# Optimization experiments

Hardware: AMD Instinct MI355X
Metric: run time of the kernel (lower is better)

Reference implementation:

```python
import jax, jax.numpy as jnp
import numpy as np

H = 16          # num heads
DH = 64         # head dim
D = H * DH      # hidden = 1024


def setup_inputs() -> dict:
    key = jax.random.key(0)
    ks = jax.random.split(key, 9)
    s = 1.0 / np.sqrt(D)
    return {
        "hidden_states": jax.random.normal(ks[0], (4, 2048, D), dtype=jnp.float32),
        "Wq": jax.random.normal(ks[1], (D, D), dtype=jnp.float32) * s,
        "bq": jax.random.normal(ks[2], (D,), dtype=jnp.float32) * 0.02,
        "Wk": jax.random.normal(ks[3], (D, D), dtype=jnp.float32) * s,
        "bk": jax.random.normal(ks[4], (D,), dtype=jnp.float32) * 0.02,
        "Wv": jax.random.normal(ks[5], (D, D), dtype=jnp.float32) * s,
        "bv": jax.random.normal(ks[6], (D,), dtype=jnp.float32) * 0.02,
        "Wo": jax.random.normal(ks[7], (D, D), dtype=jnp.float32) * s,
        "bo": jax.random.normal(ks[8], (D,), dtype=jnp.float32) * 0.02,
    }


def _split_heads(x):  # [B,S,D] -> [B,H,S,DH]
    B, S, _ = x.shape
    return x.reshape(B, S, H, DH).transpose(0, 2, 1, 3)


def reference(hidden_states, Wq, bq, Wk, bk, Wv, bv, Wo, bo):
    # torch Linear: y = x @ W.T + b  (W stored as [out, in])
    q = _split_heads(jnp.einsum('bsd,ed->bse', hidden_states, Wq) + bq)
    k = _split_heads(jnp.einsum('bsd,ed->bse', hidden_states, Wk) + bk)
    v = _split_heads(jnp.einsum('bsd,ed->bse', hidden_states, Wv) + bv)
    scores = jnp.einsum('bhqd,bhkd->bhqk', q, k) / np.sqrt(DH)
    probs = jax.nn.softmax(scores, axis=-1)  # fused softmax+matmul in original
    ctx = jnp.einsum('bhqk,bhkd->bhqd', probs, v)
    B, _, S, _ = ctx.shape
    ctx = ctx.transpose(0, 2, 1, 3).reshape(B, S, D)
    out = jnp.einsum('bsd,ed->bse', ctx, Wo) + bo
    return out  # weights are None (vis=False); dropout rate asserted 0
```

## Files before the change

kernel.cpp:

```cpp
#include <hip/hip_runtime.h>


typedef __bf16 bf16;
typedef __bf16 bf16x8 __attribute__((ext_vector_type(8)));
typedef __bf16 bf16x4 __attribute__((ext_vector_type(4)));
typedef float  floatx4 __attribute__((ext_vector_type(4)));

#define NB   4
#define SEQ  2048
#define NH   16
#define DH   64
#define DIM  1024
#define MTOT (NB * SEQ)

#define CEXP 0.18033688f

__device__ __forceinline__ floatx4 zero4() {
    floatx4 z; z[0] = 0.f; z[1] = 0.f; z[2] = 0.f; z[3] = 0.f; return z;
}

__device__ __forceinline__ void load_lds16(const bf16* g, bf16* l) {
    __builtin_amdgcn_global_load_lds(
        (__attribute__((address_space(1))) void*)g,
        (__attribute__((address_space(3))) void*)l,
        16, 0, 0);
}

__global__ __launch_bounds__(256) void cvt_all(const float* __restrict__ X,
                                               const float* __restrict__ w0,
                                               const float* __restrict__ w1,
                                               const float* __restrict__ w2,
                                               const float* __restrict__ w3,
                                               bf16* __restrict__ Xb,
                                               bf16* __restrict__ Wb) {
    const size_t MD = (size_t)MTOT * DIM;
    const size_t DD = (size_t)DIM * DIM;
    size_t i = ((size_t)blockIdx.x * 256 + threadIdx.x) * 4;
    float4 f; bf16* dst;
    if (i < MD) {
        f = *(const float4*)(X + i);
        dst = Xb + i;
    } else {
        size_t off = i - MD;
        int w = (int)(off >> 20);
        size_t wi = off & (DD - 1);
        const float* ws = (w == 0) ? w0 : (w == 1) ? w1 : (w == 2) ? w2 : w3;
        f = *(const float4*)(ws + wi);
        dst = Wb + off;
    }
    bf16x4 o;
    o[0] = (bf16)f.x; o[1] = (bf16)f.y; o[2] = (bf16)f.z; o[3] = (bf16)f.w;
    *(bf16x4*)dst = o;
}

#define QKV_TILE(T_, DO_STAGE_, WAITSTR_) do {                                 \
    const bf16* bA_ = smem + ((T_) & 3) * 16384;                               \
    const bf16* bB_ = bA_ + 8192;                                              \
    if (DO_STAGE_) {                                                           \
        bf16* sA_ = smem + (((T_) + 3) & 3) * 16384;                           \
        const int ko_ = ((T_) + 3) * 32;                                       \
        load_lds16(gA0 + ko_, sA_ + soff0);                                    \
        load_lds16(gA1 + ko_, sA_ + soff1);                                    \
        load_lds16(gB0 + ko_, sA_ + 8192 + soff0);                             \
        load_lds16(gB1 + ko_, sA_ + 8192 + soff1);                             \
    }                                                                          \
    bf16x8 afr_[4], bfg_[4];                                                   \
    _Pragma("unroll")                                                          \
    for (int mf = 0; mf < 4; mf++) afr_[mf] = *(const bf16x8*)(bA_ + aoff[mf]);\
    _Pragma("unroll")                                                          \
    for (int nf = 0; nf < 4; nf++) bfg_[nf] = *(const bf16x8*)(bB_ + boff[nf]);\
    __builtin_amdgcn_s_setprio(1);                                             \
    _Pragma("unroll")                                                          \
    for (int mf = 0; mf < 4; mf++)                                             \
        _Pragma("unroll")                                                      \
        for (int nf = 0; nf < 4; nf++)                                         \
            acc[mf][nf] = __builtin_amdgcn_mfma_f32_16x16x32_bf16(             \
                afr_[mf], bfg_[nf], acc[mf][nf], 0, 0, 0);                     \
    __builtin_amdgcn_s_setprio(0);                                             \
    _Pragma("unroll")                                                          \
    for (int mf = 0; mf < 4; mf++)                                             \
        afr_[mf] = *(const bf16x8*)(bA_ + aoff[4 + mf]);                       \
    __builtin_amdgcn_s_setprio(1);                                             \
    _Pragma("unroll")                                                          \
    for (int mf = 0; mf < 4; mf++)                                             \
        _Pragma("unroll")                                                      \
        for (int nf = 0; nf < 4; nf++)                                         \
            acc[4 + mf][nf] = __builtin_amdgcn_mfma_f32_16x16x32_bf16(         \
                afr_[mf], bfg_[nf], acc[4 + mf][nf], 0, 0, 0);                 \
    __builtin_amdgcn_s_setprio(0);                                             \
    asm volatile(WAITSTR_ ::: "memory");                                       \
    __builtin_amdgcn_s_barrier();                                              \
} while (0)

__global__ __launch_bounds__(512, 2) void gemm_qkv(const bf16* __restrict__ A,
                                                   const bf16* __restrict__ W,
                                                   const float* __restrict__ bq,
                                                   const float* __restrict__ bk,
                                                   const float* __restrict__ bv,
                                                   bf16* __restrict__ Qo,
                                                   bf16* __restrict__ Ko,
                                                   bf16* __restrict__ Vt) {
    __shared__ __align__(16) bf16 smem[4 * 16384];

    const int tid  = threadIdx.x;
    const int wave = tid >> 6, lane = tid & 63;
    const int quad = lane >> 4, l16 = lane & 15;
    const int wr = wave >> 2, wc = wave & 3;

    const int wg = (blockIdx.x & 7) * 48 + (blockIdx.x >> 3);
    const int mt = wg / 12, inner = wg % 12;
    const int sel = inner >> 2, nt = inner & 3;
    const int m0 = mt * 256, n0 = nt * 256;

    const bf16* Wsel = W + (size_t)(sel * DIM + n0) * DIM;
    const float* bias = (sel == 0) ? bq : (sel == 1) ? bk : bv;

    int aoff[8], boff[4];
#pragma unroll
    for (int mf = 0; mf < 8; mf++) {
        const int row = wr * 128 + mf * 16 + l16;
        aoff[mf] = row * 32 + ((quad ^ ((row >> 1) & 3)) * 8);
    }
#pragma unroll
    for (int nf = 0; nf < 4; nf++) {
        const int row = wc * 64 + nf * 16 + l16;
        boff[nf] = row * 32 + ((quad ^ ((row >> 1) & 3)) * 8);
    }

    const int c0 = tid, c1 = tid + 512;
    const int ra0 = c0 >> 2, qa0 = (c0 & 3) ^ ((ra0 >> 1) & 3);
    const int ra1 = c1 >> 2, qa1 = (c1 & 3) ^ ((ra1 >> 1) & 3);
    const bf16* gA0 = A + (size_t)(m0 + ra0) * DIM + qa0 * 8;
    const bf16* gA1 = A + (size_t)(m0 + ra1) * DIM + qa1 * 8;
    const bf16* gB0 = Wsel + (size_t)ra0 * DIM + qa0 * 8;
    const bf16* gB1 = Wsel + (size_t)ra1 * DIM + qa1 * 8;
    const int soff0 = (wave * 64) * 8;
    const int soff1 = (512 + wave * 64) * 8;

    floatx4 acc[8][4];
#pragma unroll
    for (int mf = 0; mf < 8; mf++)
#pragma unroll
        for (int nf = 0; nf < 4; nf++) acc[mf][nf] = zero4();

#pragma unroll
    for (int kt = 0; kt < 3; kt++) {
        bf16* sA = smem + kt * 16384;
        bf16* sB = sA + 8192;
        load_lds16(gA0 + kt * 32, sA + soff0);
        load_lds16(gA1 + kt * 32, sA + soff1);
        load_lds16(gB0 + kt * 32, sB + soff0);
        load_lds16(gB1 + kt * 32, sB + soff1);
    }
    asm volatile("s_waitcnt vmcnt(8)" ::: "memory");
    __builtin_amdgcn_s_barrier();

    const int NT = DIM / 32;
#pragma unroll 1
    for (int t = 0; t < NT - 3; t++)
        QKV_TILE(t, true, "s_waitcnt vmcnt(8)");
    QKV_TILE(NT - 3, false, "s_waitcnt vmcnt(4)");
    QKV_TILE(NT - 2, false, "s_waitcnt vmcnt(0)");
    QKV_TILE(NT - 1, false, "s_waitcnt vmcnt(0)");

    if (sel < 2) {
        bf16* C = (sel == 0) ? Qo : Ko;
        const float scale = (sel == 0) ? CEXP : 1.0f;
#pragma unroll
        for (int mf = 0; mf < 8; mf++) {
            const int rbase = m0 + wr * 128 + mf * 16 + quad * 4;
#pragma unroll
            for (int nf = 0; nf < 4; nf++) {
                const int col = n0 + wc * 64 + nf * 16 + l16;
                const float bval = bias[col];
#pragma unroll
                for (int i = 0; i < 4; i++)
                    C[(size_t)(rbase + i) * DIM + col] =
                        (bf16)((acc[mf][nf][i] + bval) * scale);
            }
        }
    } else {
        const int b  = m0 >> 11;
        const int s0 = m0 & (SEQ - 1);
#pragma unroll
        for (int mf = 0; mf < 8; mf++) {
            const int mb = wr * 128 + mf * 16 + quad * 4;
#pragma unroll
            for (int nf = 0; nf < 4; nf++) {
                const int n_loc = wc * 64 + nf * 16 + l16;
                const float bval = bias[n0 + n_loc];
                bf16x4 pk;
#pragma unroll
                for (int i = 0; i < 4; i++) pk[i] = (bf16)(acc[mf][nf][i] + bval);
                const int e = n_loc * 256 + (((mb * 2) ^ ((n_loc & 7) << 4)) >> 1);
                *(bf16x4*)(smem + e) = pk;
            }
        }
        asm volatile("s_waitcnt lgkmcnt(0)" ::: "memory");
        __builtin_amdgcn_s_barrier();
#pragma unroll
        for (int p = 0; p < 16; p++) {
            const int c = p * 512 + tid;
            const int n_loc = c >> 5, mc = (c & 31) * 8;
            const int e = n_loc * 256 + (((mc * 2) ^ ((n_loc & 7) << 4)) >> 1);
            bf16x8 v = *(const bf16x8*)(smem + e);
            const int dg = n0 + n_loc;
            const int hh = dg >> 6, d = dg & 63;
            bf16* op = Vt + ((size_t)(b * NH + hh) * DH + d) * SEQ + s0 + mc;
            *(bf16x8*)op = v;
        }
    }
}

#define OUT_TILE(T_, DO_STAGE_, WAITSTR_) do {                                 \
    const bf16* bA_ = smem + ((T_) & 3) * 12288;                               \
    const bf16* bB_ = bA_ + 8192;                                              \
    if (DO_STAGE_) {                                                           \
        bf16* sA_ = smem + (((T_) + 3) & 3) * 12288;                           \
        const int ko_ = ((T_) + 3) * 32;                                       \
        load_lds16(gA0 + ko_, sA_ + soffA0);                                   \
        load_lds16(gA1 + ko_, sA_ + soffA1);                                   \
        load_lds16(gA2 + ko_, sA_ + soffA2);                                   \
        load_lds16(gA3 + ko_, sA_ + soffA3);                                   \
        load_lds16(gB0 + ko_, sA_ + 8192 + soffB0);                            \
        load_lds16(gB1 + ko_, sA_ + 8192 + soffB1);                            \
    }                                                                          \
    bf16x8 afr_[8], bfg_[4];                                                   \
    _Pragma("unroll")                                                          \
    for (int mf = 0; mf < 8; mf++) afr_[mf] = *(const bf16x8*)(bA_ + aoff[mf]);\
    _Pragma("unroll")                                                          \
    for (int nf = 0; nf < 4; nf++) bfg_[nf] = *(const bf16x8*)(bB_ + boff[nf]);\
    __builtin_amdgcn_s_setprio(1);                                             \
    _Pragma("unroll")                                                          \
    for (int mf = 0; mf < 8; mf++)                                             \
        _Pragma("unroll")                                                      \
        for (int nf = 0; nf < 4; nf++)                                         \
            acc[mf][nf] = __builtin_amdgcn_mfma_f32_16x16x32_bf16(             \
                afr_[mf], bfg_[nf], acc[mf][nf], 0, 0, 0);                     \
    __builtin_amdgcn_s_setprio(0);                                             \
    asm volatile(WAITSTR_ ::: "memory");                                       \
    __builtin_amdgcn_s_barrier();                                              \
} while (0)

__global__ __launch_bounds__(256, 2) void gemm_out(const bf16* __restrict__ A,
                                                   const bf16* __restrict__ W,
                                                   const float* __restrict__ bias,
                                                   float* __restrict__ C) {
    __shared__ __align__(16) bf16 smem[4 * 12288];

    const int tid  = threadIdx.x;
    const int wave = tid >> 6, lane = tid & 63;
    const int quad = lane >> 4, l16 = lane & 15;
    const int wr = wave >> 1, wc = wave & 1;

    const int wg = (blockIdx.x & 7) * 32 + (blockIdx.x >> 3);
    const int mt = wg >> 3, nt = wg & 7;
    const int m0 = mt * 256, n0 = nt * 128;

    int aoff[8], boff[4];
#pragma unroll
    for (int mf = 0; mf < 8; mf++) {
        const int row = wr * 128 + mf * 16 + l16;
        aoff[mf] = row * 32 + ((quad ^ ((row >> 1) & 3)) * 8);
    }
#pragma unroll
    for (int nf = 0; nf < 4; nf++) {
        const int row = wc * 64 + nf * 16 + l16;
        boff[nf] = row * 32 + ((quad ^ ((row >> 1) & 3)) * 8);
    }

    int arow[4], aks[4];
#pragma unroll
    for (int j = 0; j < 4; j++) {
        const int c = j * 256 + tid;
        arow[j] = c >> 2; aks[j] = (c & 3) ^ ((arow[j] >> 1) & 3);
    }
    int brow[2], bks[2];
#pragma unroll
    for (int j = 0; j < 2; j++) {
        const int c = j * 256 + tid;
        brow[j] = c >> 2; bks[j] = (c & 3) ^ ((brow[j] >> 1) & 3);
    }
    const bf16* gA0 = A + (size_t)(m0 + arow[0]) * DIM + aks[0] * 8;
    const bf16* gA1 = A + (size_t)(m0 + arow[1]) * DIM + aks[1] * 8;
    const bf16* gA2 = A + (size_t)(m0 + arow[2]) * DIM + aks[2] * 8;
    const bf16* gA3 = A + (size_t)(m0 + arow[3]) * DIM + aks[3] * 8;
    const bf16* gB0 = W + (size_t)(n0 + brow[0]) * DIM + bks[0] * 8;
    const bf16* gB1 = W + (size_t)(n0 + brow[1]) * DIM + bks[1] * 8;
    const int soffA0 = (0 * 256 + wave * 64) * 8;
    const int soffA1 = (1 * 256 + wave * 64) * 8;
    const int soffA2 = (2 * 256 + wave * 64) * 8;
    const int soffA3 = (3 * 256 + wave * 64) * 8;
    const int soffB0 = (0 * 256 + wave * 64) * 8;
    const int soffB1 = (1 * 256 + wave * 64) * 8;

    floatx4 acc[8][4];
#pragma unroll
    for (int mf = 0; mf < 8; mf++)
#pragma unroll
        for (int nf = 0; nf < 4; nf++) acc[mf][nf] = zero4();

#pragma unroll
    for (int kt = 0; kt < 3; kt++) {
        bf16* sA = smem + kt * 12288;
        load_lds16(gA0 + kt * 32, sA + soffA0);
        load_lds16(gA1 + kt * 32, sA + soffA1);
        load_lds16(gA2 + kt * 32, sA + soffA2);
        load_lds16(gA3 + kt * 32, sA + soffA3);
        load_lds16(gB0 + kt * 32, sA + 8192 + soffB0);
        load_lds16(gB1 + kt * 32, sA + 8192 + soffB1);
    }
    asm volatile("s_waitcnt vmcnt(12)" ::: "memory");
    __builtin_amdgcn_s_barrier();

    const int NT = DIM / 32;
#pragma unroll 1
    for (int t = 0; t < NT - 3; t++)
        OUT_TILE(t, true, "s_waitcnt vmcnt(12)");
    OUT_TILE(NT - 3, false, "s_waitcnt vmcnt(6)");
    OUT_TILE(NT - 2, false, "s_waitcnt vmcnt(0)");
    OUT_TILE(NT - 1, false, "s_waitcnt vmcnt(0)");

#pragma unroll
    for (int mf = 0; mf < 8; mf++) {
        const int rbase = m0 + wr * 128 + mf * 16 + quad * 4;
#pragma unroll
        for (int nf = 0; nf < 4; nf++) {
            const int col = n0 + wc * 64 + nf * 16 + l16;
            const float bval = bias[col];
#pragma unroll
            for (int i = 0; i < 4; i++)
                C[(size_t)(rbase + i) * DIM + col] = acc[mf][nf][i] + bval;
        }
    }
}

#define ATTN_MFMA(A_, B_, C_) __builtin_amdgcn_mfma_f32_16x16x32_bf16(A_, B_, C_, 0, 0, 0)

#define ATTN_TILE(T_, DO_STAGE_, DO_WAIT_, WAITSTR_) do {                      \
    const int cur_ = (T_) & 3;                                                 \
    if (DO_STAGE_) {                                                           \
        const int nb_ = ((T_) + 3) & 3;                                        \
        const size_t kvn_ = (size_t)((T_) + 3) * 64;                           \
        load_lds16(kga + kvn_ * DIM, &Ks[nb_][ldsa]);                          \
        load_lds16(kgb + kvn_ * DIM, &Ks[nb_][ldsb]);                          \
        load_lds16(vga + kvn_, &Vs[nb_][ldsa]);                                \
        load_lds16(vgb + kvn_, &Vs[nb_][ldsb]);                                \
    }                                                                          \
                                                      \
    bf16x8 ke0_ = *(const bf16x8*)&Ks[cur_][koa[0]];                           \
    bf16x8 ke1_ = *(const bf16x8*)&Ks[cur_][kob[0]];                           \
    bf16x8 ko0_ = *(const bf16x8*)&Ks[cur_][koa[1]];                           \
    bf16x8 ko1_ = *(const bf16x8*)&Ks[cur_][kob[1]];                           \
    floatx4 sa0_[4], sb0_[4];                                                  \
    _Pragma("unroll")                                                          \
    for (int m = 0; m < 4; m++) {                                              \
        floatx4 sa = zero4(), sb = zero4();                                    \
        sa = ATTN_MFMA(ke0_, aq[m][0], sa);                                    \
        sa = ATTN_MFMA(ke1_, aq[m][1], sa);                                    \
        sb = ATTN_MFMA(ko0_, aq[m][0], sb);                                    \
        sb = ATTN_MFMA(ko1_, aq[m][1], sb);                                    \
        sa0_[m] = sa; sb0_[m] = sb;                                            \
    }                                                                          \
        \
    bf16x8 kf1_[4];                                                            \
    kf1_[0] = *(const bf16x8*)&Ks[cur_][koa[2]];                               \
    kf1_[1] = *(const bf16x8*)&Ks[cur_][kob[2]];                               \
    kf1_[2] = *(const bf16x8*)&Ks[cur_][koa[3]];                               \
    kf1_[3] = *(const bf16x8*)&Ks[cur_][kob[3]];                               \
    bf16x8 vf0_[4];                                                            \
    _Pragma("unroll")                                                          \
    for (int dt = 0; dt < 4; dt++)                                             \
        vf0_[dt] = *(const bf16x8*)&Vs[cur_][vo[0][dt]];                       \
                                                    \
    bf16x8 pw0_[4];                                                            \
    _Pragma("unroll")                                                          \
    for (int m = 0; m < 4; m++) {                                              \
        bf16x8 p;                                                              \
        _Pragma("unroll")                                                      \
        for (int i = 0; i < 4; i++) {                                          \
            p[i]     = (bf16)__builtin_amdgcn_exp2f(sa0_[m][i]);               \
            p[4 + i] = (bf16)__builtin_amdgcn_exp2f(sb0_[m][i]);               \
        }                                                                      \
        pw0_[m] = p;                                                           \
    }                                                                          \
                                                                   \
    floatx4 sa1_[4], sb1_[4];                                                  \
    _Pragma("unroll")                                                          \
    for (int m = 0; m < 4; m++) {                                              \
        floatx4 sa = zero4(), sb = zero4();                                    \
        sa = ATTN_MFMA(kf1_[0], aq[m][0], sa);                                 \
        sa = ATTN_MFMA(kf1_[1], aq[m][1], sa);                                 \
        sb = ATTN_MFMA(kf1_[2], aq[m][0], sb);                                 \
        sb = ATTN_MFMA(kf1_[3], aq[m][1], sb);                                 \
        sa1_[m] = sa; sb1_[m] = sb;                                            \
    }                                                                          \
                                             \
    bf16x8 vf1_[4];                                                            \
    _Pragma("unroll")                                                          \
    for (int dt = 0; dt < 4; dt++)                                             \
        vf1_[dt] = *(const bf16x8*)&Vs[cur_][vo[1][dt]];                       \
    bf16x8 pw1_[4];                                                            \
    _Pragma("unroll")                                                          \
    for (int m = 0; m < 4; m++) {                                              \
        _Pragma("unroll")                                                      \
        for (int dt = 0; dt < 4; dt++)                                         \
            acc[m][dt] = ATTN_MFMA(pw0_[m], vf0_[dt], acc[m][dt]);             \
        accl[m] = ATTN_MFMA(pw0_[m], ones8, accl[m]);                          \
        bf16x8 p;                                                              \
        _Pragma("unroll")                                                      \
        for (int i = 0; i < 4; i++) {                                          \
            p[i]     = (bf16)__builtin_amdgcn_exp2f(sa1_[m][i]);               \
            p[4 + i] = (bf16)__builtin_amdgcn_exp2f(sb1_[m][i]);               \
        }                                                                      \
        pw1_[m] = p;                                                           \
    }                                                                          \
                                                                   \
    _Pragma("unroll")                                                          \
    for (int m = 0; m < 4; m++) {                                              \
        _Pragma("unroll")                                                      \
        for (int dt = 0; dt < 4; dt++)                                         \
            acc[m][dt] = ATTN_MFMA(pw1_[m], vf1_[dt], acc[m][dt]);             \
        accl[m] = ATTN_MFMA(pw1_[m], ones8, accl[m]);                          \
    }                                                                          \
    if (DO_WAIT_) asm volatile(WAITSTR_ ::: "memory");                         \
    __builtin_amdgcn_s_barrier();                                              \
} while (0)

__global__ __launch_bounds__(256, 2) void attn_kernel(const bf16* __restrict__ Q,
                                                      const bf16* __restrict__ K,
                                                      const bf16* __restrict__ Vt,
                                                      bf16* __restrict__ Ctx) {
    __shared__ __align__(16) bf16 Ks[4][64 * 64];
    __shared__ __align__(16) bf16 Vs[4][64 * 64];

    const int tid  = threadIdx.x;
    const int wave = tid >> 6, lane = tid & 63;
    const int quad = lane >> 4, l16 = lane & 15;
    const int xcd = blockIdx.x & 7;
    const int j   = blockIdx.x >> 3;
    const int bh  = xcd * 8 + (j >> 3);
    const int qb  = j & 7;
    const int b   = bh >> 4, h = bh & 15;

    const size_t base_bh = (size_t)b * SEQ * DIM + (size_t)h * DH;
    const size_t base_v  = (size_t)bh * DH * SEQ;
    const int qt = qb * 256 + wave * 64;

    bf16x8 aq[4][2];
#pragma unroll
    for (int m = 0; m < 4; m++) {
        const bf16* qp = Q + base_bh + (size_t)(qt + m * 16 + l16) * DIM + quad * 8;
        aq[m][0] = *(const bf16x8*)qp;
        aq[m][1] = *(const bf16x8*)(qp + 32);
    }

    const int sc = wave * 128 + lane;
    int srow[2], scol[2];
    srow[0] = sc >> 3;        srow[1] = (sc + 64) >> 3;
    scol[0] = (sc & 7) ^ (srow[0] & 7);
    scol[1] = ((sc + 64) & 7) ^ (srow[1] & 7);
    auto kvloc = [](int r) {
        const int w = r >> 5, rw = r & 31, r4 = rw & 15;
        return w * 32 + ((rw >> 4) << 2) + ((r4 >> 2) << 3) + (r4 & 3);
    };
    const bf16* kga = K + base_bh + (size_t)kvloc(srow[0]) * DIM + scol[0] * 8;
    const bf16* kgb = K + base_bh + (size_t)kvloc(srow[1]) * DIM + scol[1] * 8;
    const bf16* vga = Vt + base_v + (size_t)srow[0] * SEQ + scol[0] * 8;
    const bf16* vgb = Vt + base_v + (size_t)srow[1] * SEQ + scol[1] * 8;
    const int ldsa = (wave * 128) * 8, ldsb = (wave * 128 + 64) * 8;

    int koa[4], kob[4], vo[2][4];
#pragma unroll
    for (int g = 0; g < 4; g++) {
        const int krow = g * 16 + l16;
        koa[g] = (krow * 8 + (quad ^ (krow & 7))) * 8;
        kob[g] = (krow * 8 + ((4 + quad) ^ (krow & 7))) * 8;
    }
#pragma unroll
    for (int w = 0; w < 2; w++)
#pragma unroll
        for (int dt = 0; dt < 4; dt++) {
            const int d = dt * 16 + l16;
            vo[w][dt] = d * 64 + ((4 * w + quad) ^ (d & 7)) * 8;
        }

    bf16x8 ones8;
#pragma unroll
    for (int i = 0; i < 8; i++) ones8[i] = (bf16)1.0f;

    floatx4 acc[4][4], accl[4];
#pragma unroll
    for (int m = 0; m < 4; m++) {
        accl[m] = zero4();
#pragma unroll
        for (int dt = 0; dt < 4; dt++) acc[m][dt] = zero4();
    }

#pragma unroll
    for (int kt = 0; kt < 3; kt++) {
        const size_t kvn = (size_t)kt * 64;
        load_lds16(kga + kvn * DIM, &Ks[kt][ldsa]);
        load_lds16(kgb + kvn * DIM, &Ks[kt][ldsb]);
        load_lds16(vga + kvn, &Vs[kt][ldsa]);
        load_lds16(vgb + kvn, &Vs[kt][ldsb]);
    }
    asm volatile("s_waitcnt vmcnt(8)" ::: "memory");
    __builtin_amdgcn_s_barrier();

    const int NT = SEQ / 64;
#pragma unroll 1
    for (int t = 0; t < NT - 3; t++)
        ATTN_TILE(t, true, true, "s_waitcnt vmcnt(8)");
    ATTN_TILE(NT - 3, false, true, "s_waitcnt vmcnt(4)");
    ATTN_TILE(NT - 2, false, true, "s_waitcnt vmcnt(0)");
    ATTN_TILE(NT - 1, false, false, "");

#pragma unroll
    for (int m = 0; m < 4; m++) {
        float inv[4];
#pragma unroll
        for (int i = 0; i < 4; i++) inv[i] = 1.0f / accl[m][i];
        bf16* cp = Ctx + base_bh + (size_t)(qt + m * 16 + quad * 4) * DIM + l16;
#pragma unroll
        for (int i = 0; i < 4; i++)
#pragma unroll
            for (int dt = 0; dt < 4; dt++)
                cp[(size_t)i * DIM + dt * 16] = (bf16)(acc[m][dt][i] * inv[i]);
    }
}

extern "C" void kernel_launch(void* const* d_in, const int* in_sizes, int n_in,
                              void* d_out, int out_size, void* d_ws, size_t ws_size,
                              hipStream_t stream) {
    const float* X  = (const float*)d_in[0];
    const float* Wq = (const float*)d_in[1];
    const float* bq = (const float*)d_in[2];
    const float* Wk = (const float*)d_in[3];
    const float* bk = (const float*)d_in[4];
    const float* Wv = (const float*)d_in[5];
    const float* bv = (const float*)d_in[6];
    const float* Wo = (const float*)d_in[7];
    const float* bo = (const float*)d_in[8];
    float* out = (float*)d_out;

    const size_t MD = (size_t)MTOT * DIM;
    const size_t DD = (size_t)DIM * DIM;

    bf16* Xb  = (bf16*)d_ws;
    bf16* Qb  = Xb + MD;
    bf16* Kb  = Qb + MD;
    bf16* Vtb = Kb + MD;
    bf16* Wqb = Vtb + MD;
    bf16* Wob = Wqb + 3 * DD;
    if (ws_size < (MD * 4 + DD * 4) * sizeof(bf16)) return;

    cvt_all<<<(int)((MD + 4 * DD) / 4 / 256), 256, 0, stream>>>(
        X, Wq, Wk, Wv, Wo, Xb, Wqb);

    gemm_qkv<<<384, 512, 0, stream>>>(Xb, Wqb, bq, bk, bv, Qb, Kb, Vtb);

    attn_kernel<<<NB * NH * (SEQ / 256), 256, 0, stream>>>(Qb, Kb, Vtb, Xb);

    gemm_out<<<256, 256, 0, stream>>>(Xb, Wob, bo, out);
}
```

Measured before the change: 257.2 us.

## Give each attention wave private double-buffered K/V LDS tiles, removing block barriers

Each wave now streams its own 32-key K and V tiles into a private double-buffered LDS region. It relies only on per-wave vmcnt waits, so the workgroup-wide s_barrier per tile goes away. Blocks grow to 512 threads covering 512 queries, with s_setprio raised around the MFMA sections. The aim is to stop waves stalling on each other at barriers. The cost is that every wave fetches the full K/V stream itself, multiplying global/L2 traffic. LDS use grows to 128KB per block, which limits residency to one block per CU.

After: 266.6 us. +3.7%, slower.

```diff
diff --git a/kernel.cpp b/kernel.cpp
--- a/kernel.cpp
+++ b/kernel.cpp
@@ -337,22 +337,28 @@
 
 #define ATTN_MFMA(A_, B_, C_) __builtin_amdgcn_mfma_f32_16x16x32_bf16(A_, B_, C_, 0, 0, 0)
 
-#define ATTN_TILE(T_, DO_STAGE_, DO_WAIT_, WAITSTR_) do {                      \
-    const int cur_ = (T_) & 3;                                                 \
-    if (DO_STAGE_) {                                                           \
-        const int nb_ = ((T_) + 3) & 3;                                        \
-        const size_t kvn_ = (size_t)((T_) + 3) * 64;                           \
-        load_lds16(kga + kvn_ * DIM, &Ks[nb_][ldsa]);                          \
-        load_lds16(kgb + kvn_ * DIM, &Ks[nb_][ldsb]);                          \
-        load_lds16(vga + kvn_, &Vs[nb_][ldsa]);                                \
-        load_lds16(vgb + kvn_, &Vs[nb_][ldsb]);                                \
-    }                                                                          \
-                                                      \
-    bf16x8 ke0_ = *(const bf16x8*)&Ks[cur_][koa[0]];                           \
-    bf16x8 ke1_ = *(const bf16x8*)&Ks[cur_][kob[0]];                           \
-    bf16x8 ko0_ = *(const bf16x8*)&Ks[cur_][koa[1]];                           \
-    bf16x8 ko1_ = *(const bf16x8*)&Ks[cur_][kob[1]];                           \
-    floatx4 sa0_[4], sb0_[4];                                                  \
+#define ASTAGE(T1_, NB_) do {                                                  \
+    const size_t ko_ = (size_t)(T1_) * 32 * DIM;                               \
+    const size_t vo_ = (size_t)(T1_) * 32;                                     \
+    load_lds16(kg0 + ko_, kls + (NB_) * 2048 + 0 * 512);                       \
+    load_lds16(kg1 + ko_, kls + (NB_) * 2048 + 1 * 512);                       \
+    load_lds16(kg2 + ko_, kls + (NB_) * 2048 + 2 * 512);                       \
+    load_lds16(kg3 + ko_, kls + (NB_) * 2048 + 3 * 512);                       \
+    load_lds16(vg0 + vo_, vls + (NB_) * 2048 + 0 * 512);                       \
+    load_lds16(vg1 + vo_, vls + (NB_) * 2048 + 1 * 512);                       \
+    load_lds16(vg2 + vo_, vls + (NB_) * 2048 + 2 * 512);                       \
+    load_lds16(vg3 + vo_, vls + (NB_) * 2048 + 3 * 512);                       \
+} while (0)
+
+#define ASTEP(CB_) do {                                                        \
+    const bf16* kb_ = kls + (CB_) * 2048;                                      \
+    const bf16* vb_ = vls + (CB_) * 2048;                                      \
+    bf16x8 ke0_ = *(const bf16x8*)(kb_ + koa0);                                \
+    bf16x8 ke1_ = *(const bf16x8*)(kb_ + kob0);                                \
+    bf16x8 ko0_ = *(const bf16x8*)(kb_ + koa1);                                \
+    bf16x8 ko1_ = *(const bf16x8*)(kb_ + kob1);                                \
+    floatx4 sa_[4], sb_[4];                                                    \
+    __builtin_amdgcn_s_setprio(1);                                             \
     _Pragma("unroll")                                                          \
     for (int m = 0; m < 4; m++) {                                              \
         floatx4 sa = zero4(), sb = zero4();                                    \
@@ -360,92 +366,52 @@
         sa = ATTN_MFMA(ke1_, aq[m][1], sa);                                    \
         sb = ATTN_MFMA(ko0_, aq[m][0], sb);                                    \
         sb = ATTN_MFMA(ko1_, aq[m][1], sb);                                    \
-        sa0_[m] = sa; sb0_[m] = sb;                                            \
+        sa_[m] = sa; sb_[m] = sb;                                              \
     }                                                                          \
-        \
-    bf16x8 kf1_[4];                                                            \
-    kf1_[0] = *(const bf16x8*)&Ks[cur_][koa[2]];                               \
-    kf1_[1] = *(const bf16x8*)&Ks[cur_][kob[2]];                               \
-    kf1_[2] = *(const bf16x8*)&Ks[cur_][koa[3]];                               \
-    kf1_[3] = *(const bf16x8*)&Ks[cur_][kob[3]];                               \
-    bf16x8 vf0_[4];                                                            \
-    _Pragma("unroll")                                                          \
-    for (int dt = 0; dt < 4; dt++)                                             \
-        vf0_[dt] = *(const bf16x8*)&Vs[cur_][vo[0][dt]];                       \
-                                                    \
-    bf16x8 pw0_[4];                                                            \
+    __builtin_amdgcn_s_setprio(0);                                             \
+    bf16x8 pw_[4];                                                             \
     _Pragma("unroll")                                                          \
     for (int m = 0; m < 4; m++) {                                              \
         bf16x8 p;                                                              \
         _Pragma("unroll")                                                      \
         for (int i = 0; i < 4; i++) {                                          \
-            p[i]     = (bf16)__builtin_amdgcn_exp2f(sa0_[m][i]);               \
-            p[4 + i] = (bf16)__builtin_amdgcn_exp2f(sb0_[m][i]);               \
+            p[i]     = (bf16)__builtin_amdgcn_exp2f(sa_[m][i]);                \
+            p[4 + i] = (bf16)__builtin_amdgcn_exp2f(sb_[m][i]);                \
         }                                                                      \
-        pw0_[m] = p;                                                           \
+        pw_[m] = p;                                                            \
     }                                                                          \
-                                                                   \
-    floatx4 sa1_[4], sb1_[4];                                                  \
-    _Pragma("unroll")                                                          \
-    for (int m = 0; m < 4; m++) {                                              \
-        floatx4 sa = zero4(), sb = zero4();                                    \
-        sa = ATTN_MFMA(kf1_[0], aq[m][0], sa);                                 \
-        sa = ATTN_MFMA(kf1_[1], aq[m][1], sa);                                 \
-        sb = ATTN_MFMA(kf1_[2], aq[m][0], sb);                                 \
-        sb = ATTN_MFMA(kf1_[3], aq[m][1], sb);                                 \
-        sa1_[m] = sa; sb1_[m] = sb;                                            \
-    }                                                                          \
-                                             \
-    bf16x8 vf1_[4];                                                            \
+    bf16x8 vf_[4];                                                             \
     _Pragma("unroll")                                                          \
     for (int dt = 0; dt < 4; dt++)                                             \
-        vf1_[dt] = *(const bf16x8*)&Vs[cur_][vo[1][dt]];                       \
-    bf16x8 pw1_[4];                                                            \
+        vf_[dt] = *(const bf16x8*)(vb_ + vo[dt]);                              \
+    __builtin_amdgcn_s_setprio(1);                                             \
     _Pragma("unroll")                                                          \
     for (int m = 0; m < 4; m++) {                                              \
         _Pragma("unroll")                                                      \
         for (int dt = 0; dt < 4; dt++)                                         \
-            acc[m][dt] = ATTN_MFMA(pw0_[m], vf0_[dt], acc[m][dt]);             \
-        accl[m] = ATTN_MFMA(pw0_[m], ones8, accl[m]);                          \
-        bf16x8 p;                                                              \
-        _Pragma("unroll")                                                      \
-        for (int i = 0; i < 4; i++) {                                          \
-            p[i]     = (bf16)__builtin_amdgcn_exp2f(sa1_[m][i]);               \
-            p[4 + i] = (bf16)__builtin_amdgcn_exp2f(sb1_[m][i]);               \
-        }                                                                      \
-        pw1_[m] = p;                                                           \
+            acc[m][dt] = ATTN_MFMA(pw_[m], vf_[dt], acc[m][dt]);               \
+        accl[m] = ATTN_MFMA(pw_[m], ones8, accl[m]);                           \
     }                                                                          \
-                                                                   \
-    _Pragma("unroll")                                                          \
-    for (int m = 0; m < 4; m++) {                                              \
-        _Pragma("unroll")                                                      \
-        for (int dt = 0; dt < 4; dt++)                                         \
-            acc[m][dt] = ATTN_MFMA(pw1_[m], vf1_[dt], acc[m][dt]);             \
-        accl[m] = ATTN_MFMA(pw1_[m], ones8, accl[m]);                          \
-    }                                                                          \
-    if (DO_WAIT_) asm volatile(WAITSTR_ ::: "memory");                         \
-    __builtin_amdgcn_s_barrier();                                              \
+    __builtin_amdgcn_s_setprio(0);                                             \
 } while (0)
 
-__global__ __launch_bounds__(256, 2) void attn_kernel(const bf16* __restrict__ Q,
+__global__ __launch_bounds__(512, 2) void attn_kernel(const bf16* __restrict__ Q,
                                                       const bf16* __restrict__ K,
                                                       const bf16* __restrict__ Vt,
                                                       bf16* __restrict__ Ctx) {
-    __shared__ __align__(16) bf16 Ks[4][64 * 64];
-    __shared__ __align__(16) bf16 Vs[4][64 * 64];
+    __shared__ __align__(16) bf16 KsM[8][2][32 * 64];
+    __shared__ __align__(16) bf16 VsM[8][2][64 * 32];
 
     const int tid  = threadIdx.x;
     const int wave = tid >> 6, lane = tid & 63;
     const int quad = lane >> 4, l16 = lane & 15;
-    const int xcd = blockIdx.x & 7;
-    const int j   = blockIdx.x >> 3;
-    const int bh  = xcd * 8 + (j >> 3);
-    const int qb  = j & 7;
-    const int b   = bh >> 4, h = bh & 15;
+    const int wg = (blockIdx.x & 7) * 32 + (blockIdx.x >> 3);
+    const int bh = wg >> 2, qb = wg & 3;
+    const int b  = bh >> 4, h = bh & 15;
 
     const size_t base_bh = (size_t)b * SEQ * DIM + (size_t)h * DH;
     const size_t base_v  = (size_t)bh * DH * SEQ;
-    const int qt = qb * 256 + wave * 64;
+    const int qt = qb * 512 + wave * 64;
 
     bf16x8 aq[4][2];
 #pragma unroll
@@ -455,35 +421,43 @@
         aq[m][1] = *(const bf16x8*)(qp + 32);
     }
 
-    const int sc = wave * 128 + lane;
-    int srow[2], scol[2];
-    srow[0] = sc >> 3;        srow[1] = (sc + 64) >> 3;
-    scol[0] = (sc & 7) ^ (srow[0] & 7);
-    scol[1] = ((sc + 64) & 7) ^ (srow[1] & 7);
-    auto kvloc = [](int r) {
-        const int w = r >> 5, rw = r & 31, r4 = rw & 15;
-        return w * 32 + ((rw >> 4) << 2) + ((r4 >> 2) << 3) + (r4 & 3);
-    };
-    const bf16* kga = K + base_bh + (size_t)kvloc(srow[0]) * DIM + scol[0] * 8;
-    const bf16* kgb = K + base_bh + (size_t)kvloc(srow[1]) * DIM + scol[1] * 8;
-    const bf16* vga = Vt + base_v + (size_t)srow[0] * SEQ + scol[0] * 8;
-    const bf16* vgb = Vt + base_v + (size_t)srow[1] * SEQ + scol[1] * 8;
-    const int ldsa = (wave * 128) * 8, ldsb = (wave * 128 + 64) * 8;
-
-    int koa[4], kob[4], vo[2][4];
-#pragma unroll
-    for (int g = 0; g < 4; g++) {
-        const int krow = g * 16 + l16;
-        koa[g] = (krow * 8 + (quad ^ (krow & 7))) * 8;
-        kob[g] = (krow * 8 + ((4 + quad) ^ (krow & 7))) * 8;
-    }
-#pragma unroll
-    for (int w = 0; w < 2; w++)
-#pragma unroll
-        for (int dt = 0; dt < 4; dt++) {
-            const int d = dt * 16 + l16;
-            vo[w][dt] = d * 64 + ((4 * w + quad) ^ (d & 7)) * 8;
+    const bf16 *kg0, *kg1, *kg2, *kg3;
+    {
+        const bf16* kgt[4];
+#pragma unroll
+        for (int j = 0; j < 4; j++) {
+            const int c = lane + 64 * j;
+            const int r = c >> 3, s = (c & 7) ^ (r & 7);
+            const int kv = ((r >> 4) << 2) + (((r & 15) >> 2) << 3) + (r & 3);
+            kgt[j] = K + base_bh + (size_t)kv * DIM + s * 8;
         }
+        kg0 = kgt[0]; kg1 = kgt[1]; kg2 = kgt[2]; kg3 = kgt[3];
+    }
+    const bf16 *vg0, *vg1, *vg2, *vg3;
+    {
+        const bf16* vgt[4];
+#pragma unroll
+        for (int j = 0; j < 4; j++) {
+            const int c = lane + 64 * j;
+            const int d = c >> 2, s = (c & 3) ^ (d & 3);
+            vgt[j] = Vt + base_v + (size_t)d * SEQ + s * 8;
+        }
+        vg0 = vgt[0]; vg1 = vgt[1]; vg2 = vgt[2]; vg3 = vgt[3];
+    }
+    bf16* kls = &KsM[wave][0][0];
+    bf16* vls = &VsM[wave][0][0];
+
+    const int krow0 = l16, krow1 = 16 + l16;
+    const int koa0 = (krow0 * 8 + (quad ^ (krow0 & 7))) * 8;
+    const int kob0 = (krow0 * 8 + ((4 + quad) ^ (krow0 & 7))) * 8;
+    const int koa1 = (krow1 * 8 + (quad ^ (krow1 & 7))) * 8;
+    const int kob1 = (krow1 * 8 + ((4 + quad) ^ (krow1 & 7))) * 8;
+    int vo[4];
+#pragma unroll
+    for (int dt = 0; dt < 4; dt++) {
+        const int d = dt * 16 + l16;
+        vo[dt] = d * 32 + (quad ^ (d & 3)) * 8;
+    }
 
     bf16x8 ones8;
 #pragma unroll
@@ -497,24 +471,23 @@
         for (int dt = 0; dt < 4; dt++) acc[m][dt] = zero4();
     }
 
-#pragma unroll
-    for (int kt = 0; kt < 3; kt++) {
-        const size_t kvn = (size_t)kt * 64;
-        load_lds16(kga + kvn * DIM, &Ks[kt][ldsa]);
-        load_lds16(kgb + kvn * DIM, &Ks[kt][ldsb]);
-        load_lds16(vga + kvn, &Vs[kt][ldsa]);
-        load_lds16(vgb + kvn, &Vs[kt][ldsb]);
-    }
+    ASTAGE(0, 0);
+
+    const int NT = SEQ / 32;
+#pragma unroll 1
+    for (int t = 0; t < NT - 2; t += 2) {
+        ASTAGE(t + 1, 1);
+        asm volatile("s_waitcnt vmcnt(8)" ::: "memory");
+        ASTEP(0);
+        ASTAGE(t + 2, 0);
+        asm volatile("s_waitcnt vmcnt(8)" ::: "memory");
+        ASTEP(1);
+    }
+    ASTAGE(NT - 1, 1);
     asm volatile("s_waitcnt vmcnt(8)" ::: "memory");
-    __builtin_amdgcn_s_barrier();
-
-    const int NT = SEQ / 64;
-#pragma unroll 1
-    for (int t = 0; t < NT - 3; t++)
-        ATTN_TILE(t, true, true, "s_waitcnt vmcnt(8)");
-    ATTN_TILE(NT - 3, false, true, "s_waitcnt vmcnt(4)");
-    ATTN_TILE(NT - 2, false, true, "s_waitcnt vmcnt(0)");
-    ATTN_TILE(NT - 1, false, false, "");
+    ASTEP(0);
+    asm volatile("s_waitcnt vmcnt(0)" ::: "memory");
+    ASTEP(1);
 
 #pragma unroll
     for (int m = 0; m < 4; m++) {
@@ -560,7 +533,7 @@
 
     gemm_qkv<<<384, 512, 0, stream>>>(Xb, Wqb, bq, bk, bv, Qb, Kb, Vtb);
 
-    attn_kernel<<<NB * NH * (SEQ / 256), 256, 0, stream>>>(Qb, Kb, Vtb, Xb);
+    attn_kernel<<<NB * NH * (SEQ / 512), 512, 0, stream>>>(Qb, Kb, Vtb, Xb);
 
     gemm_out<<<256, 256, 0, stream>>>(Xb, Wob, bo, out);
 }
```
